# Kernel tuning notes

Hardware: AMD Instinct MI355X
Metric: run time of the kernel (lower is better)

## Reference

```python
import jax, jax.numpy as jnp
import numpy as np

BN_EPS = 1e-5


def setup_inputs() -> dict:
    key = jax.random.key(0)
    ks = jax.random.split(key, 12)
    B, N, S, D1, D2 = 2, 16384, 4096, 128, 256
    C1, C2 = 256, 128  # mlp channels
    return {
        "xyz1": jax.random.normal(ks[0], (B, 3, N), dtype=jnp.float32),
        "xyz2": jax.random.normal(ks[1], (B, 3, S), dtype=jnp.float32),
        "points1": jax.random.normal(ks[2], (B, D1, N), dtype=jnp.float32),
        "points2": jax.random.normal(ks[3], (B, D2, S), dtype=jnp.float32),
        "w1": jax.random.normal(ks[4], (D1 + D2, C1), dtype=jnp.float32) * 0.05,
        "b1": jax.random.normal(ks[5], (C1,), dtype=jnp.float32) * 0.05,
        "g1": jax.random.uniform(ks[6], (C1,), dtype=jnp.float32, minval=0.5, maxval=1.5),
        "beta1": jax.random.normal(ks[7], (C1,), dtype=jnp.float32) * 0.05,
        "w2": jax.random.normal(ks[8], (C1, C2), dtype=jnp.float32) * 0.05,
        "b2": jax.random.normal(ks[9], (C2,), dtype=jnp.float32) * 0.05,
        "g2": jax.random.uniform(ks[10], (C2,), dtype=jnp.float32, minval=0.5, maxval=1.5),
        "beta2": jax.random.normal(ks[11], (C2,), dtype=jnp.float32) * 0.05,
    }


def _conv_bn_relu(x, W, b, g, beta):
    # 1x1 Conv1d == per-point matmul; BatchNorm1d training-mode stats over (B, N).
    y = x @ W + b                              # [B, N, Cout]
    mu = jnp.mean(y, axis=(0, 1))
    var = jnp.var(y, axis=(0, 1))              # biased variance, matches torch BN
    y = g * (y - mu) * jax.lax.rsqrt(var + BN_EPS) + beta
    return jax.nn.relu(y)


def reference(xyz1, xyz2, points1, points2, w1, b1, g1, beta1, w2, b2, g2, beta2):
    x1 = jnp.transpose(xyz1, (0, 2, 1))        # [B, N, 3]
    x2 = jnp.transpose(xyz2, (0, 2, 1))        # [B, S, 3]
    p2 = jnp.transpose(points2, (0, 2, 1))     # [B, S, D2]

    # squared pairwise distance [B, N, S], clamped at 0
    d = (jnp.sum(x1 ** 2, axis=-1, keepdims=True)
         - 2.0 * jnp.einsum('bnc,bsc->bns', x1, x2)
         + jnp.sum(x2 ** 2, axis=-1)[:, None, :])
    d = jnp.maximum(d, 0.0)

    # 3 nearest neighbors (ascending smallest distances) -- same math as full sort + slice
    neg_d3, idx = jax.lax.top_k(-d, 3)         # [B, N, 3]
    d3 = jnp.maximum(-neg_d3, 1e-6)
    recip = 1.0 / d3
    w = recip / jnp.maximum(jnp.sum(recip, axis=-1, keepdims=True), 1e-6)

    nb = jax.vmap(lambda p, i: p[i])(p2, idx)  # [B, N, 3, D2]
    interp = jnp.sum(nb * w[..., None], axis=2)
    interp = jnp.nan_to_num(interp, nan=0.0, posinf=0.0, neginf=0.0)

    p1 = jnp.transpose(points1, (0, 2, 1))     # [B, N, D1]
    x = jnp.concatenate([p1, interp], axis=-1) # [B, N, D1+D2]

    x = _conv_bn_relu(x, w1, b1, g1, beta1)
    x = _conv_bn_relu(x, w2, b2, g2, beta2)
    x = jnp.nan_to_num(x, nan=0.0, posinf=0.0, neginf=0.0)
    return jnp.transpose(x, (0, 2, 1))         # [B, C2, N]
```

## Files before the change

kernel.cpp:

```cpp
#include <hip/hip_runtime.h>

#define B_   2
#define N_   16384
#define S_   4096
#define D1_  128
#define D2_  256
#define C1_  256
#define C2_  128
#define M_   (B_ * N_)

typedef __bf16 bf16_t;
typedef bf16_t bf16x8 __attribute__((ext_vector_type(8)));
typedef float  f32x4  __attribute__((ext_vector_type(4)));

__device__ __forceinline__ void gload16(const void* g, void* l) {
  __builtin_amdgcn_global_load_lds(
      (const __attribute__((address_space(1))) void*)g,
      (__attribute__((address_space(3))) void*)l, 16, 0, 0);
}

__device__ __forceinline__ float4 cand4(const float* __restrict__ X2, int i) {
  float x = X2[i], y = X2[S_ + i], z = X2[2 * S_ + i];
  float w = fmaf(x, x, fmaf(y, y, z * z));
  return make_float4(-2.f * x, -2.f * y, -2.f * z, w);
}
__device__ __forceinline__ float distv(float4 c, float ax, float ay, float az) {
  return fmaf(ax, c.x, fmaf(ay, c.y, fmaf(az, c.z, c.w)));
}
#define TRACK3(v)                                                        \
  {                                                                      \
    float t0_ = fminf((v), m0);                                          \
    float t1_ = fminf(fmaxf((v), m0), m1);                               \
    float t2_ = fminf(fmaxf((v), m1), m2);                               \
    m0 = t0_; m1 = t1_; m2 = t2_;                                        \
  }

union SMem1 {
  struct { float4 cbuf[1024]; float T3V[2][3][32]; float QMv[32][3]; } knn;
  float tile[2][32][33];
};

__global__ __launch_bounds__(512, 8) void phase1_k(const float* __restrict__ xyz1,
                                                   const float* __restrict__ xyz2,
                                                   const float* __restrict__ points1,
                                                   const float* __restrict__ w1,
                                                   const float* __restrict__ w2,
                                                   float* __restrict__ kw,
                                                   int* __restrict__ ki,
                                                   bf16_t* __restrict__ Xp1,
                                                   bf16_t* __restrict__ w1at,
                                                   bf16_t* __restrict__ w2t) {
  __shared__ SMem1 sm;
  int bi = blockIdx.x, t = threadIdx.x;
  if (bi < 1024) {
    int l = t & 63, w = t >> 6;
    int q = l & 31, h = l >> 5;
    int s = w * 2 + h;
    int b  = bi >> 9;
    int nb = (bi & 511) * 32;
    int n  = nb + q;
    const float* X1 = xyz1 + (size_t)b * 3 * N_;
    const float* X2 = xyz2 + (size_t)b * 3 * S_;
    float ax = X1[n], ay = X1[N_ + n], az = X1[2 * N_ + n];
    float p = fmaf(ax, ax, fmaf(ay, ay, az * az));
    float m0 = 3e38f, m1 = 3e38f, m2 = 3e38f;
    for (int r = 0; r < 4; ++r) {
      __syncthreads();
      sm.knn.cbuf[t]       = cand4(X2, r * 1024 + t);
      sm.knn.cbuf[t + 512] = cand4(X2, r * 1024 + t + 512);
      __syncthreads();
      const float4* cs = sm.knn.cbuf + s * 64;
#pragma unroll 8
      for (int i = 0; i < 64; ++i) {
        float v = distv(cs[i], ax, ay, az);
        TRACK3(v);
      }
    }
    __syncthreads();
    float* SV = (float*)sm.knn.cbuf;
    SV[(s * 3 + 0) * 32 + q] = m0;  SV[(s * 3 + 1) * 32 + q] = m1;  SV[(s * 3 + 2) * 32 + q] = m2;
    __syncthreads();
    if (t < 64) {
      int th = t >> 5, tq = t & 31;
      float m0 = 3e38f, m1 = 3e38f, m2 = 3e38f;
      for (int s2 = th * 8; s2 < th * 8 + 8; ++s2)
#pragma unroll
        for (int k = 0; k < 3; ++k) {
          float v = SV[(s2 * 3 + k) * 32 + tq];
          TRACK3(v);
        }
      sm.knn.T3V[th][0][tq] = m0; sm.knn.T3V[th][1][tq] = m1; sm.knn.T3V[th][2][tq] = m2;
    }
    __syncthreads();
    float g0 = 3e38f, g1 = 3e38f, g2 = 3e38f;
    if (t < 32) {
      float m0 = sm.knn.T3V[0][0][t], m1 = sm.knn.T3V[0][1][t], m2 = sm.knn.T3V[0][2][t];
#pragma unroll
      for (int k = 0; k < 3; ++k) {
        float v = sm.knn.T3V[1][k][t];
        TRACK3(v);
      }
      g0 = m0; g1 = m1; g2 = m2;
      sm.knn.QMv[t][0] = m0; sm.knn.QMv[t][1] = m1; sm.knn.QMv[t][2] = m2;
    }
    __syncthreads();
    float q0v = sm.knn.QMv[q][0], q1v = sm.knn.QMv[q][1], q2v = sm.knn.QMv[q][2];
    unsigned j0 = 0xFFFFFFFFu, j1 = 0xFFFFFFFFu, j2 = 0xFFFFFFFFu;
    for (int r = 0; r < 4; ++r) {
      __syncthreads();
      sm.knn.cbuf[t]       = cand4(X2, r * 1024 + t);
      sm.knn.cbuf[t + 512] = cand4(X2, r * 1024 + t + 512);
      __syncthreads();
      const float4* cs = sm.knn.cbuf + s * 64;
      int base = r * 1024 + s * 64;
#pragma unroll
      for (int g = 0; g < 16; ++g) {
        float v0 = distv(cs[g * 4 + 0], ax, ay, az);
        float v1 = distv(cs[g * 4 + 1], ax, ay, az);
        float v2 = distv(cs[g * 4 + 2], ax, ay, az);
        float v3 = distv(cs[g * 4 + 3], ax, ay, az);
        float gm = fminf(fminf(v0, v1), fminf(v2, v3));
        if (gm <= q2v) {
#define CHK(vv, uu)                                                      \
          {                                                              \
            unsigned idx = (unsigned)(base + g * 4 + uu);                \
            bool h0 = ((vv) == q0v) && (j0 == 0xFFFFFFFFu);              \
            bool h1 = ((vv) == q1v) && (j1 == 0xFFFFFFFFu) && !h0;       \
            bool h2 = ((vv) == q2v) && (j2 == 0xFFFFFFFFu) && !h0 && !h1;\
            if (h0) j0 = idx;                                            \
            if (h1) j1 = idx;                                            \
            if (h2) j2 = idx;                                            \
          }
          CHK(v0, 0) CHK(v1, 1) CHK(v2, 2) CHK(v3, 3)
#undef CHK
        }
      }
    }
    __syncthreads();
    unsigned* SI = (unsigned*)sm.knn.cbuf;
    SI[(s * 3 + 0) * 32 + q] = j0;  SI[(s * 3 + 1) * 32 + q] = j1;  SI[(s * 3 + 2) * 32 + q] = j2;
    __syncthreads();
    if (t < 32) {
      unsigned a0 = 0xFFFFFFFFu, a1 = 0xFFFFFFFFu, a2 = 0xFFFFFFFFu;
      for (int s2 = 0; s2 < 16; ++s2) {
        a0 = min(a0, SI[(s2 * 3 + 0) * 32 + t]);
        a1 = min(a1, SI[(s2 * 3 + 1) * 32 + t]);
        a2 = min(a2, SI[(s2 * 3 + 2) * 32 + t]);
      }
      a0 = min(a0, (unsigned)(S_ - 1));
      a1 = min(a1, (unsigned)(S_ - 1));
      a2 = min(a2, (unsigned)(S_ - 1));
      float d0 = fmaxf(p + g0, 1e-6f);
      float d1 = fmaxf(p + g1, 1e-6f);
      float d2 = fmaxf(p + g2, 1e-6f);
      float r0 = 1.f / d0, r1 = 1.f / d1, r2 = 1.f / d2;
      float dn = fmaxf(r0 + r1 + r2, 1e-6f);
      size_t rr = (size_t)b * N_ + n;
      kw[rr * 3 + 0] = r0 / dn;  kw[rr * 3 + 1] = r1 / dn;  kw[rr * 3 + 2] = r2 / dn;
      ki[rr * 3 + 0] = (int)a0;  ki[rr * 3 + 1] = (int)a1;  ki[rr * 3 + 2] = (int)a2;
    }
  } else if (bi < 3072) {
    int bj = bi - 1024;
    int b = bj >> 10, rest = bj & 1023;
    int n0 = (rest & 255) * 64, c0 = (rest >> 8) * 32;
    int tx = t & 31, ty = (t >> 5) & 7, th = t >> 8;
    const float* src = points1 + (size_t)b * D1_ * N_;
#pragma unroll
    for (int k = 0; k < 4; ++k)
      sm.tile[th][ty + k * 8][tx] = src[(size_t)(c0 + ty + k * 8) * N_ + n0 + th * 32 + tx];
    __syncthreads();
#pragma unroll
    for (int k = 0; k < 4; ++k)
      Xp1[(size_t)(b * N_ + n0 + th * 32 + ty + k * 8) * 128 + c0 + tx] =
          (bf16_t)sm.tile[th][tx][ty + k * 8];
  } else {
    int i = (bi - 3072) * 512 + t;
    if (i < 32768) {
      int n = i >> 7, k = i & 127;
      w1at[i] = (bf16_t)w1[(size_t)k * C1_ + n];
    } else {
      int j = i - 32768;
      int n = j >> 8, k = j & 255;
      w2t[j] = (bf16_t)w2[(size_t)k * C2_ + n];
    }
  }
}

__global__ __launch_bounds__(512) void gemmG_k(const float* __restrict__ points2,
                                               const float* __restrict__ w1,
                                               bf16_t* __restrict__ G) {
  const int LDP = 40;
  __shared__ bf16_t As[128 * LDP];
  __shared__ bf16_t Bs[256 * LDP];
  int t = threadIdx.x, lane = t & 63, w = t >> 6;
  int wr = w >> 2, wc = w & 3;
  int bb = blockIdx.x >> 5;
  int m0 = (blockIdx.x & 31) * 128;
  const float* P2 = points2 + (size_t)bb * D2_ * S_;
  f32x4 acc[4][4];
  f32x4 z = {0.f, 0.f, 0.f, 0.f};
#pragma unroll
  for (int i = 0; i < 4; ++i)
#pragma unroll
    for (int j = 0; j < 4; ++j) acc[i][j] = z;
  int sA = t & 127, kgA = t >> 7;
  int nB = t & 255, kgB = t >> 8;
  for (int k0 = 0; k0 < 256; k0 += 32) {
    __syncthreads();
    {
      bf16x8 ap;
#pragma unroll
      for (int kk = 0; kk < 8; ++kk)
        ap[kk] = (bf16_t)P2[(size_t)(k0 + kgA * 8 + kk) * S_ + m0 + sA];
      *(bf16x8*)&As[sA * LDP + kgA * 8] = ap;
      bf16x8 bp0, bp1;
#pragma unroll
      for (int kk = 0; kk < 8; ++kk) {
        bp0[kk] = (bf16_t)w1[(size_t)(128 + k0 + kgB * 16 + kk) * C1_ + nB];
        bp1[kk] = (bf16_t)w1[(size_t)(128 + k0 + kgB * 16 + 8 + kk) * C1_ + nB];
      }
      *(bf16x8*)&Bs[nB * LDP + kgB * 16] = bp0;
      *(bf16x8*)&Bs[nB * LDP + kgB * 16 + 8] = bp1;
    }
    __syncthreads();
    bf16x8 af[4], bfr[4];
    int arow = wr * 64 + (lane & 15);
    int brow = wc * 64 + (lane & 15);
    int kc = 8 * (lane >> 4);
#pragma unroll
    for (int i = 0; i < 4; ++i) af[i]  = *(const bf16x8*)&As[(arow + i * 16) * LDP + kc];
#pragma unroll
    for (int j = 0; j < 4; ++j) bfr[j] = *(const bf16x8*)&Bs[(brow + j * 16) * LDP + kc];
#pragma unroll
    for (int i = 0; i < 4; ++i)
#pragma unroll
      for (int j = 0; j < 4; ++j)
        acc[i][j] = __builtin_amdgcn_mfma_f32_16x16x32_bf16(af[i], bfr[j], acc[i][j], 0, 0, 0);
  }
  bf16_t* Gb = G + (size_t)bb * S_ * 256;
#pragma unroll
  for (int j = 0; j < 4; ++j) {
    int col = wc * 64 + j * 16 + (lane & 15);
#pragma unroll
    for (int i = 0; i < 4; ++i) {
      int r = m0 + wr * 64 + i * 16 + ((lane >> 4) << 2);
#pragma unroll
      for (int q = 0; q < 4; ++q)
        Gb[(size_t)(r + q) * 256 + col] = (bf16_t)acc[i][j][q];
    }
  }
}

__global__ __launch_bounds__(256) void gemm1_k(const bf16_t* __restrict__ A,
                                               const bf16_t* __restrict__ Bt,
                                               const float* __restrict__ bias,
                                               const bf16_t* __restrict__ G,
                                               const float* __restrict__ KW,
                                               const int* __restrict__ KI,
                                               bf16_t* __restrict__ Y,
                                               float* __restrict__ st) {
  const int K = 128;
  __shared__ bf16_t As[128 * 32];
  __shared__ bf16_t Bs[128 * 32];
  int tid = threadIdx.x, lane = tid & 63, w = tid >> 6;
  int wr = w >> 1, wc = w & 1;
  int m0 = blockIdx.x * 128, n0 = blockIdx.y * 128;
  int e0 = (w * 2 + 0) * 512 + lane * 8;
  int e1 = (w * 2 + 1) * 512 + lane * 8;
  int ra0 = e0 >> 5, ca0 = e0 & 31;
  int ra1 = e1 >> 5, ca1 = e1 & 31;
  f32x4 acc[4][4];
  f32x4 z = {0.f, 0.f, 0.f, 0.f};
#pragma unroll
  for (int i = 0; i < 4; ++i)
#pragma unroll
    for (int j = 0; j < 4; ++j) acc[i][j] = z;
  for (int k0 = 0; k0 < K; k0 += 32) {
    __syncthreads();
    gload16(A + (size_t)(m0 + ra0) * K + k0 + ca0, &As[e0]);
    gload16(A + (size_t)(m0 + ra1) * K + k0 + ca1, &As[e1]);
    gload16(Bt + (size_t)(n0 + ra0) * K + k0 + ca0, &Bs[e0]);
    gload16(Bt + (size_t)(n0 + ra1) * K + k0 + ca1, &Bs[e1]);
    __syncthreads();
    bf16x8 af[4], bfr[4];
    int arow = wr * 64 + (lane & 15);
    int brow = wc * 64 + (lane & 15);
    int kc = 8 * (lane >> 4);
#pragma unroll
    for (int i = 0; i < 4; ++i) af[i]  = *(const bf16x8*)&As[(arow + i * 16) * 32 + kc];
#pragma unroll
    for (int j = 0; j < 4; ++j) bfr[j] = *(const bf16x8*)&Bs[(brow + j * 16) * 32 + kc];
#pragma unroll
    for (int i = 0; i < 4; ++i)
#pragma unroll
      for (int j = 0; j < 4; ++j)
        acc[i][j] = __builtin_amdgcn_mfma_f32_16x16x32_bf16(af[i], bfr[j], acc[i][j], 0, 0, 0);
  }
  __syncthreads();
  float* kwls = (float*)As;
  int*   kils = ((int*)As) + 384;
  if (tid < 128) {
    int r = m0 + tid;
    kwls[tid * 3 + 0] = KW[(size_t)r * 3 + 0];
    kwls[tid * 3 + 1] = KW[(size_t)r * 3 + 1];
    kwls[tid * 3 + 2] = KW[(size_t)r * 3 + 2];
    kils[tid * 3 + 0] = KI[(size_t)r * 3 + 0];
    kils[tid * 3 + 1] = KI[(size_t)r * 3 + 1];
    kils[tid * 3 + 2] = KI[(size_t)r * 3 + 2];
  }
  __syncthreads();
  int bb = m0 >> 14;
  const bf16_t* Gb = G + (size_t)bb * S_ * 256;
  float sjv[4]  = {0.f, 0.f, 0.f, 0.f};
  float ssjv[4] = {0.f, 0.f, 0.f, 0.f};
#pragma unroll
  for (int i = 0; i < 4; ++i) {
#pragma unroll
    for (int qq = 0; qq < 4; ++qq) {
      int rl = wr * 64 + i * 16 + ((lane >> 4) << 2) + qq;
      float w0 = kwls[rl * 3 + 0], w1v = kwls[rl * 3 + 1], w2v = kwls[rl * 3 + 2];
      const bf16_t* g0 = Gb + (size_t)kils[rl * 3 + 0] * 256;
      const bf16_t* g1 = Gb + (size_t)kils[rl * 3 + 1] * 256;
      const bf16_t* g2 = Gb + (size_t)kils[rl * 3 + 2] * 256;
      int r = m0 + rl;
#pragma unroll
      for (int j = 0; j < 4; ++j) {
        int col = n0 + wc * 64 + j * 16 + (lane & 15);
        float y = acc[i][j][qq] + bias[col]
                + w0 * (float)g0[col] + w1v * (float)g1[col] + w2v * (float)g2[col];
        Y[(size_t)r * C1_ + col] = (bf16_t)y;
        sjv[j] += y;  ssjv[j] += y * y;
      }
    }
  }
#pragma unroll
  for (int j = 0; j < 4; ++j) {
    float sj = sjv[j], ssj = ssjv[j];
    sj  += __shfl_xor(sj, 16);  sj  += __shfl_xor(sj, 32);
    ssj += __shfl_xor(ssj, 16); ssj += __shfl_xor(ssj, 32);
    if ((lane >> 4) == 0) {
      int col = n0 + wc * 64 + j * 16 + (lane & 15);
      atomicAdd(&st[col], sj);
      atomicAdd(&st[C1_ + col], ssj);
    }
  }
}

__global__ __launch_bounds__(256) void gemm2_k(const bf16_t* __restrict__ Y1,
                                               const bf16_t* __restrict__ Bt,
                                               const float* __restrict__ bias,
                                               const float* __restrict__ st1,
                                               const float* __restrict__ g1v,
                                               const float* __restrict__ be1,
                                               float* __restrict__ OUT,
                                               float* __restrict__ st2) {
  const int K = 256;
  __shared__ bf16_t As[128 * 32];
  __shared__ bf16_t Bs[128 * 32];
  __shared__ float sa1[C1_], sb1[C1_];
  int tid = threadIdx.x, lane = tid & 63, w = tid >> 6;
  int wr = w >> 1, wc = w & 1;
  int m0 = blockIdx.x * 128;
  {
    const float invM = 1.f / (float)M_;
    float mu  = st1[tid] * invM;
    float var = fmaxf(st1[C1_ + tid] * invM - mu * mu, 0.f);
    float a = g1v[tid] * rsqrtf(var + 1e-5f);
    sa1[tid] = a;
    sb1[tid] = be1[tid] - mu * a;
  }
  int e0 = (w * 2 + 0) * 512 + lane * 8;
  int e1 = (w * 2 + 1) * 512 + lane * 8;
  int ra0 = e0 >> 5, ca0 = e0 & 31;
  int ra1 = e1 >> 5, ca1 = e1 & 31;
  f32x4 acc[4][4];
  f32x4 z = {0.f, 0.f, 0.f, 0.f};
#pragma unroll
  for (int i = 0; i < 4; ++i)
#pragma unroll
    for (int j = 0; j < 4; ++j) acc[i][j] = z;
  bf16x8 va0 = *(const bf16x8*)&Y1[(size_t)(m0 + ra0) * C1_ + ca0];
  bf16x8 va1 = *(const bf16x8*)&Y1[(size_t)(m0 + ra1) * C1_ + ca1];
  __syncthreads();
  for (int k0 = 0; k0 < K; k0 += 32) {
    bf16x8 nb0, nb1;
    if (k0 + 32 < K) {
      nb0 = *(const bf16x8*)&Y1[(size_t)(m0 + ra0) * C1_ + k0 + 32 + ca0];
      nb1 = *(const bf16x8*)&Y1[(size_t)(m0 + ra1) * C1_ + k0 + 32 + ca1];
    }
    if (k0) __syncthreads();
    bf16x8 oa0, oa1;
#pragma unroll
    for (int u = 0; u < 8; ++u) {
      float f0 = (float)va0[u];
      float f1 = (float)va1[u];
      f0 = fmaxf(f0 * sa1[k0 + ca0 + u] + sb1[k0 + ca0 + u], 0.f);
      f1 = fmaxf(f1 * sa1[k0 + ca1 + u] + sb1[k0 + ca1 + u], 0.f);
      oa0[u] = (bf16_t)f0;
      oa1[u] = (bf16_t)f1;
    }
    *(bf16x8*)&As[e0] = oa0;
    *(bf16x8*)&As[e1] = oa1;
    gload16(Bt + (size_t)ra0 * K + k0 + ca0, &Bs[e0]);
    gload16(Bt + (size_t)ra1 * K + k0 + ca1, &Bs[e1]);
    __syncthreads();
    bf16x8 af[4], bfr[4];
    int arow = wr * 64 + (lane & 15);
    int brow = wc * 64 + (lane & 15);
    int kc = 8 * (lane >> 4);
#pragma unroll
    for (int i = 0; i < 4; ++i) af[i]  = *(const bf16x8*)&As[(arow + i * 16) * 32 + kc];
#pragma unroll
    for (int j = 0; j < 4; ++j) bfr[j] = *(const bf16x8*)&Bs[(brow + j * 16) * 32 + kc];
#pragma unroll
    for (int i = 0; i < 4; ++i)
#pragma unroll
      for (int j = 0; j < 4; ++j)
        acc[i][j] = __builtin_amdgcn_mfma_f32_16x16x32_bf16(af[i], bfr[j], acc[i][j], 0, 0, 0);
    va0 = nb0; va1 = nb1;
  }
#pragma unroll
  for (int j = 0; j < 4; ++j) {
    int col = wc * 64 + j * 16 + (lane & 15);
    float bv = bias[col];
    float sj = 0.f, ssj = 0.f;
#pragma unroll
    for (int i = 0; i < 4; ++i) {
      int r  = m0 + wr * 64 + i * 16 + ((lane >> 4) << 2);
      int bb = r >> 14, n = r & (N_ - 1);
      f32x4 v = acc[i][j];
#pragma unroll
      for (int q = 0; q < 4; ++q) {
        v[q] += bv;
        sj += v[q]; ssj += v[q] * v[q];
      }
      *(f32x4*)&OUT[((size_t)(bb * C2_ + col)) * N_ + n] = v;
    }
    sj  += __shfl_xor(sj, 16);  sj  += __shfl_xor(sj, 32);
    ssj += __shfl_xor(ssj, 16); ssj += __shfl_xor(ssj, 32);
    if ((lane >> 4) == 0) {
      atomicAdd(&st2[col], sj);
      atomicAdd(&st2[C2_ + col], ssj);
    }
  }
}

__global__ __launch_bounds__(256) void bn2apply_k(float* __restrict__ OUT,
                                                  const float* __restrict__ st,
                                                  const float* __restrict__ g,
                                                  const float* __restrict__ be) {
  __shared__ float ab[2];
  int t = threadIdx.x;
  int c = (blockIdx.x >> 4) & 127;
  if (t == 0) {
    const float invM = 1.f / (float)M_;
    float mu  = st[c] * invM;
    float var = fmaxf(st[C2_ + c] * invM - mu * mu, 0.f);
    float a = g[c] * rsqrtf(var + 1e-5f);
    ab[0] = a;
    ab[1] = be[c] - mu * a;
  }
  __syncthreads();
  float a = ab[0], s = ab[1];
  size_t i4 = (size_t)blockIdx.x * 256 + t;
  f32x4 v = *(f32x4*)&OUT[i4 * 4];
#pragma unroll
  for (int u = 0; u < 4; ++u) v[u] = fmaxf(a * v[u] + s, 0.f);
  *(f32x4*)&OUT[i4 * 4] = v;
}

extern "C" void kernel_launch(void* const* d_in, const int* in_sizes, int n_in,
                              void* d_out, int out_size, void* d_ws, size_t ws_size,
                              hipStream_t stream) {
  const float* xyz1    = (const float*)d_in[0];
  const float* xyz2    = (const float*)d_in[1];
  const float* points1 = (const float*)d_in[2];
  const float* points2 = (const float*)d_in[3];
  const float* w1      = (const float*)d_in[4];
  const float* b1      = (const float*)d_in[5];
  const float* g1      = (const float*)d_in[6];
  const float* beta1   = (const float*)d_in[7];
  const float* w2      = (const float*)d_in[8];
  const float* b2      = (const float*)d_in[9];
  const float* g2      = (const float*)d_in[10];
  const float* beta2   = (const float*)d_in[11];
  float* out = (float*)d_out;

  char* p = (char*)d_ws;
  size_t off = 0;
  bf16_t* Xp1  = (bf16_t*)(p + off); off += (size_t)M_ * 128 * 2;
  bf16_t* W1AT = (bf16_t*)(p + off); off += (size_t)C1_ * 128 * 2;
  bf16_t* W2T  = (bf16_t*)(p + off); off += (size_t)C2_ * C1_ * 2;
  bf16_t* G    = (bf16_t*)(p + off); off += (size_t)B_ * S_ * 256 * 2;
  bf16_t* Y1   = (bf16_t*)(p + off); off += (size_t)M_ * C1_ * 2;
  float*  KW   = (float*)(p + off);  off += (size_t)M_ * 3 * 4;
  int*    KI   = (int*)(p + off);    off += (size_t)M_ * 3 * 4;
  float*  ST1  = (float*)(p + off);  off += 2048;
  float*  ST2  = (float*)(p + off);  off += 1024;

  hipMemsetAsync(ST1, 0, 3072, stream);

  phase1_k<<<3200, 512, 0, stream>>>(xyz1, xyz2, points1, w1, w2,
                                     KW, KI, Xp1, W1AT, W2T);
  gemmG_k<<<64, 512, 0, stream>>>(points2, w1, G);
  gemm1_k<<<dim3(M_ / 128, 2), 256, 0, stream>>>(Xp1, W1AT, b1, G, KW, KI, Y1, ST1);
  gemm2_k<<<M_ / 128, 256, 0, stream>>>(Y1, W2T, b2, ST1, g1, beta1, out, ST2);
  bn2apply_k<<<4096, 256, 0, stream>>>(out, ST2, g2, beta2);
}
```

Baseline: 135.5 us.

## Fold G GEMM into phase1, use med3 in kNN, shrink gemm2 tiles

Several changes land at once. The separate points2×W1b GEMM kernel is folded into phase1_k as 128 extra blocks with 128x128 tiles, which removes one kernel launch and lets this work overlap with the kNN blocks. The kNN top-3 tracking now uses the v_med3_f32 instruction in place of fmin/fmax pairs, and its inner loop unroll goes from 8 to 16. gemm2 tiles shrink from 128 to 64 rows with launch bounds set for 3 blocks per CU, doubling the grid to improve occupancy, at the cost of more redundant B-tile loads and more atomic stat updates.

```diff
diff --git a/kernel.cpp b/kernel.cpp
--- a/kernel.cpp
+++ b/kernel.cpp
@@ -19,6 +19,12 @@
       (__attribute__((address_space(3))) void*)l, 16, 0, 0);
 }
 
+__device__ __forceinline__ float med3a(float a, float b, float c) {
+  float d;
+  asm("v_med3_f32 %0, %1, %2, %3" : "=v"(d) : "v"(a), "v"(b), "v"(c));
+  return d;
+}
+
 __device__ __forceinline__ float4 cand4(const float* __restrict__ X2, int i) {
   float x = X2[i], y = X2[S_ + i], z = X2[2 * S_ + i];
   float w = fmaf(x, x, fmaf(y, y, z * z));
@@ -30,26 +36,29 @@
 #define TRACK3(v)                                                        \
   {                                                                      \
     float t0_ = fminf((v), m0);                                          \
-    float t1_ = fminf(fmaxf((v), m0), m1);                               \
-    float t2_ = fminf(fmaxf((v), m1), m2);                               \
+    float t1_ = med3a((v), m0, m1);                                      \
+    float t2_ = med3a((v), m1, m2);                                      \
     m0 = t0_; m1 = t1_; m2 = t2_;                                        \
   }
 
 union SMem1 {
   struct { float4 cbuf[1024]; float T3V[2][3][32]; float QMv[32][3]; } knn;
+  struct { bf16_t As[128 * 32]; bf16_t Bs[128 * 32]; } gg;
   float tile[2][32][33];
 };
 
 __global__ __launch_bounds__(512, 8) void phase1_k(const float* __restrict__ xyz1,
                                                    const float* __restrict__ xyz2,
                                                    const float* __restrict__ points1,
+                                                   const float* __restrict__ points2,
                                                    const float* __restrict__ w1,
                                                    const float* __restrict__ w2,
                                                    float* __restrict__ kw,
                                                    int* __restrict__ ki,
                                                    bf16_t* __restrict__ Xp1,
                                                    bf16_t* __restrict__ w1at,
-                                                   bf16_t* __restrict__ w2t) {
+                                                   bf16_t* __restrict__ w2t,
+                                                   bf16_t* __restrict__ G) {
   __shared__ SMem1 sm;
   int bi = blockIdx.x, t = threadIdx.x;
   if (bi < 1024) {
@@ -70,7 +79,7 @@
       sm.knn.cbuf[t + 512] = cand4(X2, r * 1024 + t + 512);
       __syncthreads();
       const float4* cs = sm.knn.cbuf + s * 64;
-#pragma unroll 8
+#pragma unroll 16
       for (int i = 0; i < 64; ++i) {
         float v = distv(cs[i], ax, ay, az);
         TRACK3(v);
@@ -159,8 +168,59 @@
       kw[rr * 3 + 0] = r0 / dn;  kw[rr * 3 + 1] = r1 / dn;  kw[rr * 3 + 2] = r2 / dn;
       ki[rr * 3 + 0] = (int)a0;  ki[rr * 3 + 1] = (int)a1;  ki[rr * 3 + 2] = (int)a2;
     }
-  } else if (bi < 3072) {
-    int bj = bi - 1024;
+  } else if (bi < 1152) {
+    int idx = bi - 1024;
+    int bb = idx >> 6, rem = idx & 63;
+    int m0 = (rem >> 1) * 128, n0 = (rem & 1) * 128;
+    const float* P2 = points2 + (size_t)bb * D2_ * S_;
+    int lane = t & 63, w = t >> 6;
+    int wr = w >> 2, wc = w & 3;
+    f32x4 acc[4][2];
+    f32x4 z = {0.f, 0.f, 0.f, 0.f};
+#pragma unroll
+    for (int i = 0; i < 4; ++i) { acc[i][0] = z; acc[i][1] = z; }
+    int sA = t & 127, kg = t >> 7;
+    for (int k0 = 0; k0 < 256; k0 += 32) {
+      __syncthreads();
+      {
+        bf16x8 ap, bp;
+#pragma unroll
+        for (int kk = 0; kk < 8; ++kk) {
+          ap[kk] = (bf16_t)P2[(size_t)(k0 + kg * 8 + kk) * S_ + m0 + sA];
+          bp[kk] = (bf16_t)w1[(size_t)(128 + k0 + kg * 8 + kk) * C1_ + n0 + sA];
+        }
+        *(bf16x8*)&sm.gg.As[sA * 32 + kg * 8] = ap;
+        *(bf16x8*)&sm.gg.Bs[sA * 32 + kg * 8] = bp;
+      }
+      __syncthreads();
+      int arow = wr * 64 + (lane & 15);
+      int brow = wc * 32 + (lane & 15);
+      int kc = 8 * (lane >> 4);
+      bf16x8 bfr[2];
+#pragma unroll
+      for (int j = 0; j < 2; ++j) bfr[j] = *(const bf16x8*)&sm.gg.Bs[(brow + j * 16) * 32 + kc];
+#pragma unroll
+      for (int i = 0; i < 4; ++i) {
+        bf16x8 af = *(const bf16x8*)&sm.gg.As[(arow + i * 16) * 32 + kc];
+#pragma unroll
+        for (int j = 0; j < 2; ++j)
+          acc[i][j] = __builtin_amdgcn_mfma_f32_16x16x32_bf16(af, bfr[j], acc[i][j], 0, 0, 0);
+      }
+    }
+    bf16_t* Gb = G + (size_t)bb * S_ * 256;
+#pragma unroll
+    for (int j = 0; j < 2; ++j) {
+      int col = n0 + wc * 32 + j * 16 + (lane & 15);
+#pragma unroll
+      for (int i = 0; i < 4; ++i) {
+        int r = m0 + wr * 64 + i * 16 + ((lane >> 4) << 2);
+#pragma unroll
+        for (int q = 0; q < 4; ++q)
+          Gb[(size_t)(r + q) * 256 + col] = (bf16_t)acc[i][j][q];
+      }
+    }
+  } else if (bi < 3200) {
+    int bj = bi - 1152;
     int b = bj >> 10, rest = bj & 1023;
     int n0 = (rest & 255) * 64, c0 = (rest >> 8) * 32;
     int tx = t & 31, ty = (t >> 5) & 7, th = t >> 8;
@@ -174,7 +234,7 @@
       Xp1[(size_t)(b * N_ + n0 + th * 32 + ty + k * 8) * 128 + c0 + tx] =
           (bf16_t)sm.tile[th][tx][ty + k * 8];
   } else {
-    int i = (bi - 3072) * 512 + t;
+    int i = (bi - 3200) * 512 + t;
     if (i < 32768) {
       int n = i >> 7, k = i & 127;
       w1at[i] = (bf16_t)w1[(size_t)k * C1_ + n];
@@ -182,71 +242,6 @@
       int j = i - 32768;
       int n = j >> 8, k = j & 255;
       w2t[j] = (bf16_t)w2[(size_t)k * C2_ + n];
-    }
-  }
-}
-
-__global__ __launch_bounds__(512) void gemmG_k(const float* __restrict__ points2,
-                                               const float* __restrict__ w1,
-                                               bf16_t* __restrict__ G) {
-  const int LDP = 40;
-  __shared__ bf16_t As[128 * LDP];
-  __shared__ bf16_t Bs[256 * LDP];
-  int t = threadIdx.x, lane = t & 63, w = t >> 6;
-  int wr = w >> 2, wc = w & 3;
-  int bb = blockIdx.x >> 5;
-  int m0 = (blockIdx.x & 31) * 128;
-  const float* P2 = points2 + (size_t)bb * D2_ * S_;
-  f32x4 acc[4][4];
-  f32x4 z = {0.f, 0.f, 0.f, 0.f};
-#pragma unroll
-  for (int i = 0; i < 4; ++i)
-#pragma unroll
-    for (int j = 0; j < 4; ++j) acc[i][j] = z;
-  int sA = t & 127, kgA = t >> 7;
-  int nB = t & 255, kgB = t >> 8;
-  for (int k0 = 0; k0 < 256; k0 += 32) {
-    __syncthreads();
-    {
-      bf16x8 ap;
-#pragma unroll
-      for (int kk = 0; kk < 8; ++kk)
-        ap[kk] = (bf16_t)P2[(size_t)(k0 + kgA * 8 + kk) * S_ + m0 + sA];
-      *(bf16x8*)&As[sA * LDP + kgA * 8] = ap;
-      bf16x8 bp0, bp1;
-#pragma unroll
-      for (int kk = 0; kk < 8; ++kk) {
-        bp0[kk] = (bf16_t)w1[(size_t)(128 + k0 + kgB * 16 + kk) * C1_ + nB];
-        bp1[kk] = (bf16_t)w1[(size_t)(128 + k0 + kgB * 16 + 8 + kk) * C1_ + nB];
-      }
-      *(bf16x8*)&Bs[nB * LDP + kgB * 16] = bp0;
-      *(bf16x8*)&Bs[nB * LDP + kgB * 16 + 8] = bp1;
-    }
-    __syncthreads();
-    bf16x8 af[4], bfr[4];
-    int arow = wr * 64 + (lane & 15);
-    int brow = wc * 64 + (lane & 15);
-    int kc = 8 * (lane >> 4);
-#pragma unroll
-    for (int i = 0; i < 4; ++i) af[i]  = *(const bf16x8*)&As[(arow + i * 16) * LDP + kc];
-#pragma unroll
-    for (int j = 0; j < 4; ++j) bfr[j] = *(const bf16x8*)&Bs[(brow + j * 16) * LDP + kc];
-#pragma unroll
-    for (int i = 0; i < 4; ++i)
-#pragma unroll
-      for (int j = 0; j < 4; ++j)
-        acc[i][j] = __builtin_amdgcn_mfma_f32_16x16x32_bf16(af[i], bfr[j], acc[i][j], 0, 0, 0);
-  }
-  bf16_t* Gb = G + (size_t)bb * S_ * 256;
-#pragma unroll
-  for (int j = 0; j < 4; ++j) {
-    int col = wc * 64 + j * 16 + (lane & 15);
-#pragma unroll
-    for (int i = 0; i < 4; ++i) {
-      int r = m0 + wr * 64 + i * 16 + ((lane >> 4) << 2);
-#pragma unroll
-      for (int q = 0; q < 4; ++q)
-        Gb[(size_t)(r + q) * 256 + col] = (bf16_t)acc[i][j][q];
     }
   }
 }
@@ -346,21 +341,21 @@
   }
 }
 
-__global__ __launch_bounds__(256) void gemm2_k(const bf16_t* __restrict__ Y1,
-                                               const bf16_t* __restrict__ Bt,
-                                               const float* __restrict__ bias,
-                                               const float* __restrict__ st1,
-                                               const float* __restrict__ g1v,
-                                               const float* __restrict__ be1,
-                                               float* __restrict__ OUT,
-                                               float* __restrict__ st2) {
+__global__ __launch_bounds__(256, 3) void gemm2_k(const bf16_t* __restrict__ Y1,
+                                                  const bf16_t* __restrict__ Bt,
+                                                  const float* __restrict__ bias,
+                                                  const float* __restrict__ st1,
+                                                  const float* __restrict__ g1v,
+                                                  const float* __restrict__ be1,
+                                                  float* __restrict__ OUT,
+                                                  float* __restrict__ st2) {
   const int K = 256;
-  __shared__ bf16_t As[128 * 32];
+  __shared__ bf16_t As[64 * 32];
   __shared__ bf16_t Bs[128 * 32];
   __shared__ float sa1[C1_], sb1[C1_];
   int tid = threadIdx.x, lane = tid & 63, w = tid >> 6;
   int wr = w >> 1, wc = w & 1;
-  int m0 = blockIdx.x * 128;
+  int m0 = blockIdx.x * 64;
   {
     const float invM = 1.f / (float)M_;
     float mu  = st1[tid] * invM;
@@ -369,55 +364,46 @@
     sa1[tid] = a;
     sb1[tid] = be1[tid] - mu * a;
   }
-  int e0 = (w * 2 + 0) * 512 + lane * 8;
-  int e1 = (w * 2 + 1) * 512 + lane * 8;
-  int ra0 = e0 >> 5, ca0 = e0 & 31;
-  int ra1 = e1 >> 5, ca1 = e1 & 31;
-  f32x4 acc[4][4];
+  int ra = tid >> 2, ca = (tid & 3) * 8;
+  int rb0 = tid >> 2, rb1 = 64 + rb0;
+  f32x4 acc[2][4];
   f32x4 z = {0.f, 0.f, 0.f, 0.f};
 #pragma unroll
-  for (int i = 0; i < 4; ++i)
+  for (int i = 0; i < 2; ++i)
 #pragma unroll
     for (int j = 0; j < 4; ++j) acc[i][j] = z;
-  bf16x8 va0 = *(const bf16x8*)&Y1[(size_t)(m0 + ra0) * C1_ + ca0];
-  bf16x8 va1 = *(const bf16x8*)&Y1[(size_t)(m0 + ra1) * C1_ + ca1];
+  bf16x8 va = *(const bf16x8*)&Y1[(size_t)(m0 + ra) * C1_ + ca];
   __syncthreads();
   for (int k0 = 0; k0 < K; k0 += 32) {
-    bf16x8 nb0, nb1;
-    if (k0 + 32 < K) {
-      nb0 = *(const bf16x8*)&Y1[(size_t)(m0 + ra0) * C1_ + k0 + 32 + ca0];
-      nb1 = *(const bf16x8*)&Y1[(size_t)(m0 + ra1) * C1_ + k0 + 32 + ca1];
-    }
+    bf16x8 nv;
+    if (k0 + 32 < K)
+      nv = *(const bf16x8*)&Y1[(size_t)(m0 + ra) * C1_ + k0 + 32 + ca];
     if (k0) __syncthreads();
-    bf16x8 oa0, oa1;
+    bf16x8 oa;
 #pragma unroll
     for (int u = 0; u < 8; ++u) {
-      float f0 = (float)va0[u];
-      float f1 = (float)va1[u];
-      f0 = fmaxf(f0 * sa1[k0 + ca0 + u] + sb1[k0 + ca0 + u], 0.f);
-      f1 = fmaxf(f1 * sa1[k0 + ca1 + u] + sb1[k0 + ca1 + u], 0.f);
-      oa0[u] = (bf16_t)f0;
-      oa1[u] = (bf16_t)f1;
-    }
-    *(bf16x8*)&As[e0] = oa0;
-    *(bf16x8*)&As[e1] = oa1;
-    gload16(Bt + (size_t)ra0 * K + k0 + ca0, &Bs[e0]);
-    gload16(Bt + (size_t)ra1 * K + k0 + ca1, &Bs[e1]);
-    __syncthreads();
-    bf16x8 af[4], bfr[4];
-    int arow = wr * 64 + (lane & 15);
+      float f0 = (float)va[u];
+      f0 = fmaxf(f0 * sa1[k0 + ca + u] + sb1[k0 + ca + u], 0.f);
+      oa[u] = (bf16_t)f0;
+    }
+    *(bf16x8*)&As[ra * 32 + ca] = oa;
+    gload16(Bt + (size_t)rb0 * K + k0 + ca, &Bs[rb0 * 32 + ca]);
+    gload16(Bt + (size_t)rb1 * K + k0 + ca, &Bs[rb1 * 32 + ca]);
+    __syncthreads();
+    bf16x8 af[2], bfr[4];
+    int arow = wr * 32 + (lane & 15);
     int brow = wc * 64 + (lane & 15);
     int kc = 8 * (lane >> 4);
 #pragma unroll
-    for (int i = 0; i < 4; ++i) af[i]  = *(const bf16x8*)&As[(arow + i * 16) * 32 + kc];
+    for (int i = 0; i < 2; ++i) af[i]  = *(const bf16x8*)&As[(arow + i * 16) * 32 + kc];
 #pragma unroll
     for (int j = 0; j < 4; ++j) bfr[j] = *(const bf16x8*)&Bs[(brow + j * 16) * 32 + kc];
 #pragma unroll
-    for (int i = 0; i < 4; ++i)
+    for (int i = 0; i < 2; ++i)
 #pragma unroll
       for (int j = 0; j < 4; ++j)
         acc[i][j] = __builtin_amdgcn_mfma_f32_16x16x32_bf16(af[i], bfr[j], acc[i][j], 0, 0, 0);
-    va0 = nb0; va1 = nb1;
+    va = nv;
   }
 #pragma unroll
   for (int j = 0; j < 4; ++j) {
@@ -425,8 +411,8 @@
     float bv = bias[col];
     float sj = 0.f, ssj = 0.f;
 #pragma unroll
-    for (int i = 0; i < 4; ++i) {
-      int r  = m0 + wr * 64 + i * 16 + ((lane >> 4) << 2);
+    for (int i = 0; i < 2; ++i) {
+      int r  = m0 + wr * 32 + i * 16 + ((lane >> 4) << 2);
       int bb = r >> 14, n = r & (N_ - 1);
       f32x4 v = acc[i][j];
 #pragma unroll
@@ -500,10 +486,9 @@
 
   hipMemsetAsync(ST1, 0, 3072, stream);
 
-  phase1_k<<<3200, 512, 0, stream>>>(xyz1, xyz2, points1, w1, w2,
-                                     KW, KI, Xp1, W1AT, W2T);
-  gemmG_k<<<64, 512, 0, stream>>>(points2, w1, G);
+  phase1_k<<<3328, 512, 0, stream>>>(xyz1, xyz2, points1, points2, w1, w2,
+                                     KW, KI, Xp1, W1AT, W2T, G);
   gemm1_k<<<dim3(M_ / 128, 2), 256, 0, stream>>>(Xp1, W1AT, b1, G, KW, KI, Y1, ST1);
-  gemm2_k<<<M_ / 128, 256, 0, stream>>>(Y1, W2T, b2, ST1, g1, beta1, out, ST2);
+  gemm2_k<<<M_ / 64, 256, 0, stream>>>(Y1, W2T, b2, ST1, g1, beta1, out, ST2);
   bn2apply_k<<<4096, 256, 0, stream>>>(out, ST2, g2, beta2);
 }
```

New measurement: 138.8 us. 1.02x slower.
